# Kernel optimization log

Hardware: AMD Instinct MI355X
Metric: run time of the kernel (lower is better)

## Reference

```python
import jax, jax.numpy as jnp
import numpy as np


def setup_inputs() -> dict:
    key = jax.random.key(0)
    k1, k2, k3 = jax.random.split(key, 3)
    T, B, H = 2048, 16, 512
    inputs = jax.random.normal(k1, (T, B, H), dtype=jnp.float32)
    # torch.rand override of the context vector, made explicit/deterministic
    rand_ctx = jax.random.uniform(k2, (T, B, H), dtype=jnp.float32)
    # xavier_uniform_ with relu gain: bound = gain * sqrt(6/(fan_in+fan_out))
    gain = float(np.sqrt(2.0))
    bound = gain * float(np.sqrt(6.0 / (H + H)))
    W = jax.random.uniform(k3, (H, H), dtype=jnp.float32, minval=-bound, maxval=bound)
    return {"inputs": inputs, "rand_ctx": rand_ctx, "W": W, "attention_width": 3}


def reference(inputs, rand_ctx, W, attention_width):
    # inputs: [T, B, H]; attention_width is dead code in the original (lb=0 always)
    T, B, H = inputs.shape
    # Context half of the output: inputs[t] for t<2, random override for t>=2
    t_col = jnp.arange(T)[:, None, None]
    ctx = jnp.where(t_col < 2, inputs, rand_ctx)               # [T, B, H]
    results = jnp.concatenate([inputs, ctx], axis=-1)          # [T, B, 2H]

    # Attention weights (detached in the original, never fed to the output):
    # scores[b, t, s] = (x_t W) . x_s, softmax over s < t, only for t >= 2
    q = jnp.einsum('tbh,hk->tbk', inputs, W)                   # [T, B, H]
    scores = jnp.einsum('tbk,sbk->bts', q, inputs)             # [B, T, T]
    t_idx = jnp.arange(T)
    mask = (t_idx[None, :] < t_idx[:, None]) & (t_idx[:, None] >= 2)  # [T, T]
    neg = jnp.finfo(scores.dtype).min
    attn = jax.nn.softmax(jnp.where(mask[None], scores, neg), axis=-1)
    attn = jnp.where(mask[None], attn, jnp.zeros((), scores.dtype))   # zero padded rows
    return results, attn
```

## Files before the change

kernel.cpp:

```cpp
#include <hip/hip_runtime.h>
#include <math.h>

#define T_DIM 2048
#define B_DIM 16
#define H_DIM 512
#define NKB   (H_DIM / 32)

typedef _Float16 f16x8 __attribute__((ext_vector_type(8)));
typedef float f32x4 __attribute__((ext_vector_type(4)));

__device__ __forceinline__ unsigned short h_bits(_Float16 h) {
    unsigned short u; __builtin_memcpy(&u, &h, 2); return u;
}
__device__ __forceinline__ float h2f(unsigned short u) {
    _Float16 h; __builtin_memcpy(&h, &u, 2); return (float)h;
}

__device__ __forceinline__ size_t tile_off(int rowblk, int kblk) {
    return ((size_t)rowblk * NKB + kblk) * 4096;
}
__device__ __forceinline__ size_t tiled_idx(int r, int c) {
    return tile_off(r >> 7, c >> 5) + (size_t)((c >> 3) & 3) * 1024 + (size_t)(r & 127) * 8 + (c & 7);
}

__global__ __launch_bounds__(256) void k_prep(const float* __restrict__ X,
                                              const float* __restrict__ RC,
                                              const float* __restrict__ W,
                                              float* __restrict__ out,
                                              unsigned short* __restrict__ Xh,
                                              unsigned short* __restrict__ Wth) {
    if (blockIdx.x >= 8192) {
        int i = (blockIdx.x - 8192) * 256 + threadIdx.x;
        int n = i & 511;
        int k0 = (i >> 9) * 8;
        unsigned int hw[4];
#pragma unroll
        for (int e = 0; e < 4; ++e) {
            _Float16 h0 = (_Float16)W[(size_t)(k0 + 2 * e) * H_DIM + n];
            _Float16 h1 = (_Float16)W[(size_t)(k0 + 2 * e + 1) * H_DIM + n];
            hw[e] = (unsigned int)h_bits(h0) | ((unsigned int)h_bits(h1) << 16);
        }
        *(uint4*)(Wth + tiled_idx(n, k0)) = make_uint4(hw[0], hw[1], hw[2], hw[3]);
        return;
    }
    int i = blockIdx.x * 256 + threadIdx.x;
    int row = i >> 6;
    int h0 = (i & 63) * 8;
    int t = row >> 4;
    int b = row & 15;
    const float* xp = X + (size_t)row * H_DIM + h0;
    float4 v0 = *(const float4*)xp;
    float4 v1 = *(const float4*)(xp + 4);
    float* op = out + (size_t)row * (2 * H_DIM) + h0;
    *(float4*)op = v0;
    *(float4*)(op + 4) = v1;
    const float* cp = RC + (size_t)row * H_DIM + h0;
    float4 c0 = *(const float4*)cp;
    float4 c1 = *(const float4*)(cp + 4);
    if (t < 2) { c0 = v0; c1 = v1; }
    *(float4*)(op + H_DIM) = c0;
    *(float4*)(op + H_DIM + 4) = c1;
    float xs[8] = {v0.x, v0.y, v0.z, v0.w, v1.x, v1.y, v1.z, v1.w};
    unsigned int hw[4];
#pragma unroll
    for (int e = 0; e < 4; ++e) {
        _Float16 a = (_Float16)xs[2 * e], bb = (_Float16)xs[2 * e + 1];
        hw[e] = (unsigned int)h_bits(a) | ((unsigned int)h_bits(bb) << 16);
    }
    int r = b * T_DIM + t;
    *(uint4*)(Xh + tiled_idx(r, h0)) = make_uint4(hw[0], hw[1], hw[2], hw[3]);
}

__device__ __forceinline__ void stage_half(const unsigned short* __restrict__ src_tile,
                                           unsigned short* lds_base, int lane, int h) {
#pragma unroll
    for (int c = 0; c < 4; ++c) {
        const int ch = h * 4 + c;
        __builtin_amdgcn_global_load_lds(
            (const __attribute__((address_space(1))) void*)(src_tile + ch * 512 + lane * 8),
            (__attribute__((address_space(3))) void*)(lds_base + ch * 512),
            16, 0, 0);
    }
}

__global__ __launch_bounds__(256) void k_qgemm_mfma(const unsigned short* __restrict__ Xh,
                                                    const unsigned short* __restrict__ Wth,
                                                    unsigned short* __restrict__ Qh) {
    __shared__ __align__(16) unsigned short Ah[2][4][128][8], Bh[2][4][128][8];
    const int bid = blockIdx.x;
    const int swz = (bid & 7) * 128 + (bid >> 3);
    const int mblk = swz >> 2, nblk = swz & 3;
    const int m0 = mblk * 128, n0 = nblk * 128;
    const int tid = threadIdx.x, lane = tid & 63, w = tid >> 6;
    const int t_off = (w >> 1) * 64, s_off = (w & 1) * 64;
    const int l15 = lane & 15, lg = lane >> 4;
    f32x4 acc[4][4] = {};

    for (int ksp = 0; ksp < NKB / 2; ++ksp) {
        if (ksp) __syncthreads();
        if (w < 2) {
            stage_half(Xh + tile_off(mblk, 2 * ksp),     &Ah[0][0][0][0], lane, w);
            stage_half(Xh + tile_off(mblk, 2 * ksp + 1), &Ah[1][0][0][0], lane, w);
        } else {
            stage_half(Wth + tile_off(nblk, 2 * ksp),     &Bh[0][0][0][0], lane, w - 2);
            stage_half(Wth + tile_off(nblk, 2 * ksp + 1), &Bh[1][0][0][0], lane, w - 2);
        }
        __syncthreads();

#pragma unroll
        for (int kk = 0; kk < 2; ++kk) {
            f16x8 ah[4], bh[4];
#pragma unroll
            for (int i2 = 0; i2 < 4; ++i2)
                ah[i2] = *(const f16x8*)&Ah[kk][lg][t_off + i2 * 16 + l15][0];
#pragma unroll
            for (int j = 0; j < 4; ++j)
                bh[j] = *(const f16x8*)&Bh[kk][lg][s_off + j * 16 + l15][0];
#pragma unroll
            for (int i2 = 0; i2 < 4; ++i2)
#pragma unroll
                for (int j = 0; j < 4; ++j)
                    acc[i2][j] = __builtin_amdgcn_mfma_f32_16x16x32_f16(ah[i2], bh[j], acc[i2][j], 0, 0, 0);
        }
    }

#pragma unroll
    for (int i2 = 0; i2 < 4; ++i2)
#pragma unroll
        for (int j = 0; j < 4; ++j)
#pragma unroll
            for (int r = 0; r < 4; ++r) {
                int R = m0 + t_off + i2 * 16 + lg * 4 + r;
                int C = n0 + s_off + j * 16 + l15;
                _Float16 qh = (_Float16)acc[i2][j][r];
                Qh[tiled_idx(R, C)] = h_bits(qh);
            }
}

__global__ __launch_bounds__(256) void k_scores_mfma(const unsigned short* __restrict__ Qh,
                                                     const unsigned short* __restrict__ Xh,
                                                     float* __restrict__ attn) {
    const int bid = blockIdx.x;
    const int swz = (bid & 7) * 272 + (bid >> 3);
    const int b = swz / 136;
    const int r = swz - b * 136;
    int ti = (int)((sqrtf(8.f * (float)r + 1.f) - 1.f) * 0.5f);
    while ((ti + 1) * (ti + 2) / 2 <= r) ++ti;
    while (ti * (ti + 1) / 2 > r) --ti;
    const int si = r - ti * (ti + 1) / 2;
    const int t0 = ti * 128, s0 = si * 128;

    __shared__ __align__(16) unsigned short Ah[2][4][128][8], Bh[2][4][128][8];
    const int tid = threadIdx.x, lane = tid & 63, w = tid >> 6;
    const int t_off = (w >> 1) * 64, s_off = (w & 1) * 64;
    const int l15 = lane & 15, lg = lane >> 4;
    const int ablk = b * (T_DIM / 128) + ti;
    const int bblk = b * (T_DIM / 128) + si;
    f32x4 acc[4][4] = {};

    for (int ksp = 0; ksp < NKB / 2; ++ksp) {
        if (ksp) __syncthreads();
        if (w < 2) {
            stage_half(Qh + tile_off(ablk, 2 * ksp),     &Ah[0][0][0][0], lane, w);
            stage_half(Qh + tile_off(ablk, 2 * ksp + 1), &Ah[1][0][0][0], lane, w);
        } else {
            stage_half(Xh + tile_off(bblk, 2 * ksp),     &Bh[0][0][0][0], lane, w - 2);
            stage_half(Xh + tile_off(bblk, 2 * ksp + 1), &Bh[1][0][0][0], lane, w - 2);
        }
        __syncthreads();

#pragma unroll
        for (int kk = 0; kk < 2; ++kk) {
            f16x8 ah[4], bh[4];
#pragma unroll
            for (int i2 = 0; i2 < 4; ++i2)
                ah[i2] = *(const f16x8*)&Ah[kk][lg][t_off + i2 * 16 + l15][0];
#pragma unroll
            for (int j = 0; j < 4; ++j)
                bh[j] = *(const f16x8*)&Bh[kk][lg][s_off + j * 16 + l15][0];
#pragma unroll
            for (int i2 = 0; i2 < 4; ++i2)
#pragma unroll
                for (int j = 0; j < 4; ++j)
                    acc[i2][j] = __builtin_amdgcn_mfma_f32_16x16x32_f16(ah[i2], bh[j], acc[i2][j], 0, 0, 0);
        }
    }

    float* base = attn + (size_t)b * T_DIM * T_DIM;
#pragma unroll
    for (int i2 = 0; i2 < 4; ++i2)
#pragma unroll
        for (int j = 0; j < 4; ++j)
#pragma unroll
            for (int rr = 0; rr < 4; ++rr) {
                int t = t0 + t_off + i2 * 16 + lg * 4 + rr;
                int s = s0 + s_off + j * 16 + l15;
                _Float16 hv = (_Float16)acc[i2][j][rr];
                ((unsigned short*)(base + (size_t)t * T_DIM))[s] = h_bits(hv);
            }
}

__global__ __launch_bounds__(256) void k_softmax(float* __restrict__ attn) {
    const int row = blockIdx.x;
    const int t = row & (T_DIM - 1);
    float* p = attn + (size_t)row * T_DIM;
    const int tid = threadIdx.x;
    const int n = (t >= 2) ? t : 0;
    __shared__ float redm[4], redl[4];

    if (n == 0) {
        const float4 z = {0.f, 0.f, 0.f, 0.f};
        *(float4*)&p[tid * 8] = z;
        *(float4*)&p[tid * 8 + 4] = z;
        return;
    }

    const int sbase = tid * 8;
    uint4 rv = *(const uint4*)((const unsigned short*)p + sbase);
    float v[8];
    v[0] = h2f((unsigned short)(rv.x & 0xffff)); v[1] = h2f((unsigned short)(rv.x >> 16));
    v[2] = h2f((unsigned short)(rv.y & 0xffff)); v[3] = h2f((unsigned short)(rv.y >> 16));
    v[4] = h2f((unsigned short)(rv.z & 0xffff)); v[5] = h2f((unsigned short)(rv.z >> 16));
    v[6] = h2f((unsigned short)(rv.w & 0xffff)); v[7] = h2f((unsigned short)(rv.w >> 16));

    float m = -1e30f, l = 0.f;
#pragma unroll
    for (int j = 0; j < 8; ++j)
        if (sbase + j < n) m = fmaxf(m, v[j]);
#pragma unroll
    for (int j = 0; j < 8; ++j)
        if (sbase + j < n) l += expf(v[j] - m);

#pragma unroll
    for (int off = 1; off <= 32; off <<= 1) {
        float mo = __shfl_xor(m, off);
        float lo = __shfl_xor(l, off);
        float M = fmaxf(m, mo);
        l = l * expf(m - M) + lo * expf(mo - M);
        m = M;
    }
    if ((tid & 63) == 0) { redm[tid >> 6] = m; redl[tid >> 6] = l; }
    __syncthreads();
    {
        float M = fmaxf(fmaxf(redm[0], redm[1]), fmaxf(redm[2], redm[3]));
        float L = redl[0] * expf(redm[0] - M) + redl[1] * expf(redm[1] - M)
                + redl[2] * expf(redm[2] - M) + redl[3] * expf(redm[3] - M);
        m = M;
        l = L;
    }
    const float inv = 1.f / l;

    float o[8];
#pragma unroll
    for (int j = 0; j < 8; ++j)
        o[j] = (sbase + j < n) ? expf(v[j] - m) * inv : 0.f;
    float4 o0 = {o[0], o[1], o[2], o[3]};
    float4 o1 = {o[4], o[5], o[6], o[7]};
    *(float4*)&p[sbase] = o0;
    *(float4*)&p[sbase + 4] = o1;
}

extern "C" void kernel_launch(void* const* d_in, const int* in_sizes, int n_in,
                              void* d_out, int out_size, void* d_ws, size_t ws_size,
                              hipStream_t stream) {
    const float* inputs   = (const float*)d_in[0];
    const float* rand_ctx = (const float*)d_in[1];
    const float* W        = (const float*)d_in[2];
    float* out  = (float*)d_out;
    float* attn = out + (size_t)T_DIM * B_DIM * 2 * H_DIM;

    unsigned short* Xh  = (unsigned short*)d_ws;
    unsigned short* Qh  = Xh + (size_t)33554432;
    unsigned short* Wth = Xh + (size_t)67108864;

    k_prep<<<dim3(8192 + 128), dim3(256), 0, stream>>>(
        inputs, rand_ctx, W, out, Xh, Wth);

    k_qgemm_mfma<<<dim3(1024), dim3(256), 0, stream>>>(Xh, Wth, Qh);

    k_scores_mfma<<<dim3(2176), dim3(256), 0, stream>>>(Qh, Xh, attn);

    k_softmax<<<dim3(B_DIM * T_DIM), dim3(256), 0, stream>>>(attn);
}
```

Baseline: 293.6 us.

## Widen scores GEMM tile to 128x256 over causal lower-triangle blocks

Each block of the scores kernel now computes a 128x256 output tile instead of 128x128, with every wave holding a 64x128 accumulator (4x8 MFMA tiles). The triangular block enumeration is rewritten for 256-wide column pairs, which cuts the grid from 2176 to 1152 blocks. Each staged Q tile is now reused across twice as many columns, reducing global and LDS traffic per FLOP. In exchange, accumulator register use doubles, which may lower occupancy, and some tiles on the diagonal compute columns that are not needed.

```diff
diff --git a/kernel.cpp b/kernel.cpp
--- a/kernel.cpp
+++ b/kernel.cpp
@@ -82,6 +82,16 @@
             16, 0, 0);
     }
 }
+__device__ __forceinline__ void stage_chunks(const unsigned short* __restrict__ src_tile,
+                                             unsigned short* lds_base, int lane,
+                                             int c0, int c1) {
+    for (int c = c0; c < c1; ++c) {
+        __builtin_amdgcn_global_load_lds(
+            (const __attribute__((address_space(1))) void*)(src_tile + c * 512 + lane * 8),
+            (__attribute__((address_space(3))) void*)(lds_base + c * 512),
+            16, 0, 0);
+    }
+}
 
 __global__ __launch_bounds__(256) void k_qgemm_mfma(const unsigned short* __restrict__ Xh,
                                                     const unsigned short* __restrict__ Wth,
@@ -141,47 +151,59 @@
                                                      const unsigned short* __restrict__ Xh,
                                                      float* __restrict__ attn) {
     const int bid = blockIdx.x;
-    const int swz = (bid & 7) * 272 + (bid >> 3);
-    const int b = swz / 136;
-    const int r = swz - b * 136;
-    int ti = (int)((sqrtf(8.f * (float)r + 1.f) - 1.f) * 0.5f);
-    while ((ti + 1) * (ti + 2) / 2 <= r) ++ti;
-    while (ti * (ti + 1) / 2 > r) --ti;
-    const int si = r - ti * (ti + 1) / 2;
-    const int t0 = ti * 128, s0 = si * 128;
-
-    __shared__ __align__(16) unsigned short Ah[2][4][128][8], Bh[2][4][128][8];
+    const int swz = (bid & 7) * 144 + (bid >> 3);
+    const int b = swz / 72;
+    int r = swz - b * 72;
+    int ti = 0;
+    for (;; ++ti) {
+        const int c = (ti + 2) >> 1;
+        if (r < c) break;
+        r -= c;
+    }
+    const int si2 = r;
+    const int t0 = ti * 128, s0 = si2 * 256;
+
+    __shared__ __align__(16) unsigned short S[6 * 4096];
     const int tid = threadIdx.x, lane = tid & 63, w = tid >> 6;
-    const int t_off = (w >> 1) * 64, s_off = (w & 1) * 64;
+    const int wr = w >> 1, wc = w & 1;
     const int l15 = lane & 15, lg = lane >> 4;
-    const int ablk = b * (T_DIM / 128) + ti;
-    const int bblk = b * (T_DIM / 128) + si;
-    f32x4 acc[4][4] = {};
+    const int ablk  = b * (T_DIM / 128) + ti;
+    const int bblk0 = b * (T_DIM / 128) + si2 * 2;
+    f32x4 acc[4][8] = {};
 
     for (int ksp = 0; ksp < NKB / 2; ++ksp) {
         if (ksp) __syncthreads();
-        if (w < 2) {
-            stage_half(Qh + tile_off(ablk, 2 * ksp),     &Ah[0][0][0][0], lane, w);
-            stage_half(Qh + tile_off(ablk, 2 * ksp + 1), &Ah[1][0][0][0], lane, w);
-        } else {
-            stage_half(Xh + tile_off(bblk, 2 * ksp),     &Bh[0][0][0][0], lane, w - 2);
-            stage_half(Xh + tile_off(bblk, 2 * ksp + 1), &Bh[1][0][0][0], lane, w - 2);
+        {
+            const unsigned short* A0  = Qh + tile_off(ablk, 2 * ksp);
+            const unsigned short* A1  = Qh + tile_off(ablk, 2 * ksp + 1);
+            const unsigned short* B00 = Xh + tile_off(bblk0, 2 * ksp);
+            const unsigned short* B01 = Xh + tile_off(bblk0, 2 * ksp + 1);
+            const unsigned short* B10 = Xh + tile_off(bblk0 + 1, 2 * ksp);
+            const unsigned short* B11 = Xh + tile_off(bblk0 + 1, 2 * ksp + 1);
+            if      (w == 0) { stage_chunks(A0,  S,            lane, 0, 8);
+                               stage_chunks(A1,  S + 4096,     lane, 0, 4); }
+            else if (w == 1) { stage_chunks(A1,  S + 4096,     lane, 4, 8);
+                               stage_chunks(B00, S + 2 * 4096, lane, 0, 8); }
+            else if (w == 2) { stage_chunks(B01, S + 3 * 4096, lane, 0, 8);
+                               stage_chunks(B10, S + 4 * 4096, lane, 0, 4); }
+            else             { stage_chunks(B10, S + 4 * 4096, lane, 4, 8);
+                               stage_chunks(B11, S + 5 * 4096, lane, 0, 8); }
         }
         __syncthreads();
 
 #pragma unroll
         for (int kk = 0; kk < 2; ++kk) {
-            f16x8 ah[4], bh[4];
+            f16x8 ah[4], bh[8];
 #pragma unroll
             for (int i2 = 0; i2 < 4; ++i2)
-                ah[i2] = *(const f16x8*)&Ah[kk][lg][t_off + i2 * 16 + l15][0];
-#pragma unroll
-            for (int j = 0; j < 4; ++j)
-                bh[j] = *(const f16x8*)&Bh[kk][lg][s_off + j * 16 + l15][0];
+                ah[i2] = *(const f16x8*)&S[kk * 4096 + (lg * 128 + wr * 64 + i2 * 16 + l15) * 8];
+#pragma unroll
+            for (int j = 0; j < 8; ++j)
+                bh[j] = *(const f16x8*)&S[(2 + wc * 2 + kk) * 4096 + (lg * 128 + j * 16 + l15) * 8];
 #pragma unroll
             for (int i2 = 0; i2 < 4; ++i2)
 #pragma unroll
-                for (int j = 0; j < 4; ++j)
+                for (int j = 0; j < 8; ++j)
                     acc[i2][j] = __builtin_amdgcn_mfma_f32_16x16x32_f16(ah[i2], bh[j], acc[i2][j], 0, 0, 0);
         }
     }
@@ -190,11 +212,11 @@
 #pragma unroll
     for (int i2 = 0; i2 < 4; ++i2)
 #pragma unroll
-        for (int j = 0; j < 4; ++j)
+        for (int j = 0; j < 8; ++j)
 #pragma unroll
             for (int rr = 0; rr < 4; ++rr) {
-                int t = t0 + t_off + i2 * 16 + lg * 4 + rr;
-                int s = s0 + s_off + j * 16 + l15;
+                int t = t0 + wr * 64 + i2 * 16 + lg * 4 + rr;
+                int s = s0 + wc * 128 + j * 16 + l15;
                 _Float16 hv = (_Float16)acc[i2][j][rr];
                 ((unsigned short*)(base + (size_t)t * T_DIM))[s] = h_bits(hv);
             }
@@ -278,7 +300,7 @@
 
     k_qgemm_mfma<<<dim3(1024), dim3(256), 0, stream>>>(Xh, Wth, Qh);
 
-    k_scores_mfma<<<dim3(2176), dim3(256), 0, stream>>>(Qh, Xh, attn);
+    k_scores_mfma<<<dim3(1152), dim3(256), 0, stream>>>(Qh, Xh, attn);
 
     k_softmax<<<dim3(B_DIM * T_DIM), dim3(256), 0, stream>>>(attn);
 }
```

Result: slower. 318.0 us (+8.3%).
